# Kernel tuning notes

Hardware: AMD Instinct MI355X
Metric: run time of the kernel (lower is better)

Reference implementation:

```python
import jax, jax.numpy as jnp
import numpy as np

N = 50000
E = 800000
D_IN = 128
D_EMB = 128
D_OUT = 2
AGGRS = ('sum', 'max', 'mean', 'sum', 'max', 'mean')


def setup_inputs() -> dict:
    key = jax.random.key(0)
    ks = jax.random.split(key, 10)
    x = jax.random.normal(ks[0], (N, D_IN), dtype=jnp.float32)
    edge_index = jax.random.randint(ks[1], (2, E), 0, N, dtype=jnp.int64)
    # 6 SAGEConv layers, all 128->128: lin_l (weight+bias, applied to aggregated
    # neighbors) and lin_r (weight only, applied to root/self features).
    w_l = jax.random.normal(ks[2], (6, D_EMB, D_EMB), dtype=jnp.float32) * 0.05
    b_l = jax.random.normal(ks[3], (6, D_EMB), dtype=jnp.float32) * 0.05
    w_r = jax.random.normal(ks[4], (6, D_EMB, D_EMB), dtype=jnp.float32) * 0.05
    w1 = jax.random.normal(ks[5], (D_EMB, D_EMB), dtype=jnp.float32) * 0.05
    b1 = jax.random.normal(ks[6], (D_EMB,), dtype=jnp.float32) * 0.05
    w2 = jax.random.normal(ks[7], (D_EMB, D_OUT), dtype=jnp.float32) * 0.05
    b2 = jax.random.normal(ks[8], (D_OUT,), dtype=jnp.float32) * 0.05
    return {"x": x, "edge_index": edge_index, "w_l": w_l, "b_l": b_l,
            "w_r": w_r, "w1": w1, "b1": b1, "w2": w2, "b2": b2}


def _aggregate(msg, dst, aggr, num_nodes):
    # msg: [E, D] gathered source features; dst: [E] target node ids.
    if aggr == 'sum':
        return jax.ops.segment_sum(msg, dst, num_segments=num_nodes)
    if aggr == 'max':
        m = jax.ops.segment_max(msg, dst, num_segments=num_nodes)
        # nodes with no incoming edges -> 0 (PyG scatter-max fill)
        return jnp.where(jnp.isfinite(m), m, 0.0)
    # mean
    s = jax.ops.segment_sum(msg, dst, num_segments=num_nodes)
    cnt = jax.ops.segment_sum(jnp.ones((msg.shape[0],), msg.dtype), dst,
                              num_segments=num_nodes)
    return s / jnp.maximum(cnt, 1.0)[:, None]


def _sage_conv(x, src, dst, wl, bl, wr, aggr):
    msg = x[src]                               # [E, D] gather
    agg = _aggregate(msg, dst, aggr, x.shape[0])
    return agg @ wl + bl + x @ wr              # lin_l(aggr) + lin_r(x)


def reference(x, edge_index, w_l, b_l, w_r, w1, b1, w2, b2):
    src, dst = edge_index[0], edge_index[1]    # messages flow src -> dst
    h = x
    for i, aggr in enumerate(AGGRS):
        h = _sage_conv(h, src, dst, w_l[i], b_l[i], w_r[i], aggr)
        h = jax.nn.relu(h)                     # dropout p=0.1 is identity in eval
    h = jax.nn.relu(h @ w1 + b1)
    return h @ w2 + b2
```

## Files before the change

kernel.cpp:

```cpp
#include <hip/hip_runtime.h>

#define NN 50000
#define NE 800000
#define D 128

typedef unsigned short ushort_t;
typedef __attribute__((ext_vector_type(8))) short short8;
typedef __attribute__((ext_vector_type(4))) float f32x4;
typedef __attribute__((ext_vector_type(8))) _Float16 half8;
typedef __attribute__((ext_vector_type(2))) _Float16 half2v;


__global__ void k_hist(const int* __restrict__ dst, int* __restrict__ cnt, int e) {
  int i = blockIdx.x * blockDim.x + threadIdx.x;
  if (i < e) atomicAdd(&cnt[dst[i]], 1);
}

__global__ __launch_bounds__(1024) void k_scan(const int* __restrict__ cnt,
                                               int* __restrict__ row_start,
                                               int* __restrict__ cursor, int n) {
  __shared__ int wsum[16];
  __shared__ int carry_s;
  int t = threadIdx.x;
  int lane = t & 63, wid = t >> 6;
  if (t == 0) carry_s = 0;
  __syncthreads();
  for (int base = 0; base < n; base += 4096) {
    int i = base + t * 4;
    int4 v = make_int4(0, 0, 0, 0);
    if (i + 3 < n) v = *(const int4*)&cnt[i];
    else if (i < n) {
      v.x = cnt[i];
      if (i + 1 < n) v.y = cnt[i + 1];
      if (i + 2 < n) v.z = cnt[i + 2];
    }
    int tot = v.x + v.y + v.z + v.w;
    int x = tot;
    #pragma unroll
    for (int off = 1; off < 64; off <<= 1) {
      int y = __shfl_up(x, off, 64);
      if (lane >= off) x += y;
    }
    if (lane == 63) wsum[wid] = x;
    __syncthreads();
    if (wid == 0) {
      int w = (lane < 16) ? wsum[lane] : 0;
      #pragma unroll
      for (int off = 1; off < 16; off <<= 1) {
        int y = __shfl_up(w, off, 64);
        if (lane >= off) w += y;
      }
      if (lane < 16) wsum[lane] = w;
    }
    __syncthreads();
    int off0 = carry_s + (wid ? wsum[wid - 1] : 0) + (x - tot);
    int4 o;
    o.x = off0;
    o.y = off0 + v.x;
    o.z = off0 + v.x + v.y;
    o.w = off0 + v.x + v.y + v.z;
    if (i + 3 < n) {
      *(int4*)&row_start[i] = o;
      *(int4*)&cursor[i] = o;
    } else if (i < n) {
      row_start[i] = o.x; cursor[i] = o.x;
      if (i + 1 < n) { row_start[i + 1] = o.y; cursor[i + 1] = o.y; }
      if (i + 2 < n) { row_start[i + 2] = o.z; cursor[i + 2] = o.z; }
    }
    __syncthreads();
    if (t == 0) carry_s += wsum[15];
    __syncthreads();
  }
  if (t == 0) row_start[n] = carry_s;
}

__global__ __launch_bounds__(256) void k_scatter(const int* __restrict__ src,
                                                 const int* __restrict__ dst,
                                                 int* __restrict__ cursor,
                                                 int* __restrict__ csr_src, int e) {
  int i = (blockIdx.x * 256 + threadIdx.x) * 4;
  if (i >= e) return;
  int4 s4 = *(const int4*)&src[i];
  int4 d4 = *(const int4*)&dst[i];
  int p0 = atomicAdd(&cursor[d4.x], 1);
  int p1 = atomicAdd(&cursor[d4.y], 1);
  int p2 = atomicAdd(&cursor[d4.z], 1);
  int p3 = atomicAdd(&cursor[d4.w], 1);
  csr_src[p0] = s4.x;
  csr_src[p1] = s4.y;
  csr_src[p2] = s4.z;
  csr_src[p3] = s4.w;
}


__global__ __launch_bounds__(256) void k_tofp16(const float* __restrict__ in,
                                                _Float16* __restrict__ out, int n8) {
  int i = blockIdx.x * 256 + threadIdx.x;
  if (i >= n8) return;
  float4 a = ((const float4*)in)[i * 2];
  float4 b = ((const float4*)in)[i * 2 + 1];
  half8 o;
  o[0] = (_Float16)a.x; o[1] = (_Float16)a.y; o[2] = (_Float16)a.z; o[3] = (_Float16)a.w;
  o[4] = (_Float16)b.x; o[5] = (_Float16)b.y; o[6] = (_Float16)b.z; o[7] = (_Float16)b.w;
  ((half8*)out)[i] = o;
}


__global__ void k_wsplit(const float* __restrict__ W, ushort_t* __restrict__ hi,
                         ushort_t* __restrict__ lo, int total) {
  int idx = blockIdx.x * 256 + threadIdx.x;
  if (idx >= total) return;
  int mat = idx >> 14, rem = idx & 16383;
  int k = rem >> 7, c = rem & 127;
  float f = W[idx];
  unsigned u = __float_as_uint(f);
  float lf = f - __uint_as_float(u & 0xffff0000u);
  size_t dst = ((size_t)mat << 14) + (size_t)(k >> 5) * 4096 + c * 32 + (k & 31);
  hi[dst] = (ushort_t)(u >> 16);
  lo[dst] = (ushort_t)(__float_as_uint(lf) >> 16);
}


__device__ __forceinline__ float4 op_add(float4 a, float4 v) {
  a.x += v.x; a.y += v.y; a.z += v.z; a.w += v.w; return a;
}
__device__ __forceinline__ float4 op_max(float4 a, float4 v) {
  a.x = fmaxf(a.x, v.x); a.y = fmaxf(a.y, v.y);
  a.z = fmaxf(a.z, v.z); a.w = fmaxf(a.w, v.w); return a;
}
__device__ __forceinline__ void h8_to_f(half8 v, float4& x, float4& y) {
  x.x = (float)v[0]; x.y = (float)v[1]; x.z = (float)v[2]; x.w = (float)v[3];
  y.x = (float)v[4]; y.y = (float)v[5]; y.z = (float)v[6]; y.w = (float)v[7];
}

template <int AGGR>
__global__ __launch_bounds__(256) void k_aggregate(const _Float16* __restrict__ h,
                                                   const int* __restrict__ csr_src,
                                                   const int* __restrict__ row_start,
                                                   _Float16* __restrict__ agg, int n) {
  int lane = threadIdx.x & 63;
  int node = blockIdx.x * 4 + (threadIdx.x >> 6);
  if (node >= n) return;
  int slot = lane >> 4, c = lane & 15;
  const half8* __restrict__ hp = (const half8*)h;
  int s = row_start[node], e = row_start[node + 1];
  float4 init;
  if (AGGR == 1) init = make_float4(-INFINITY, -INFINITY, -INFINITY, -INFINITY);
  else           init = make_float4(0.f, 0.f, 0.f, 0.f);
  float4 a0x = init, a0y = init, a1x = init, a1y = init;
  int j = s + slot;
  for (; j + 4 < e; j += 8) {
    int i0 = csr_src[j], i1 = csr_src[j + 4];
    half8 v0 = hp[(size_t)i0 * 16 + c];
    half8 v1 = hp[(size_t)i1 * 16 + c];
    float4 v0x, v0y, v1x, v1y;
    h8_to_f(v0, v0x, v0y);
    h8_to_f(v1, v1x, v1y);
    if (AGGR == 1) {
      a0x = op_max(a0x, v0x); a0y = op_max(a0y, v0y);
      a1x = op_max(a1x, v1x); a1y = op_max(a1y, v1y);
    } else {
      a0x = op_add(a0x, v0x); a0y = op_add(a0y, v0y);
      a1x = op_add(a1x, v1x); a1y = op_add(a1y, v1y);
    }
  }
  for (; j < e; j += 4) {
    half8 v0 = hp[(size_t)csr_src[j] * 16 + c];
    float4 v0x, v0y;
    h8_to_f(v0, v0x, v0y);
    if (AGGR == 1) { a0x = op_max(a0x, v0x); a0y = op_max(a0y, v0y); }
    else           { a0x = op_add(a0x, v0x); a0y = op_add(a0y, v0y); }
  }
  float4 rx, ry;
  if (AGGR == 1) { rx = op_max(a0x, a1x); ry = op_max(a0y, a1y); }
  else           { rx = op_add(a0x, a1x); ry = op_add(a0y, a1y); }
  #pragma unroll
  for (int off = 16; off <= 32; off <<= 1) {
    float4 ox, oy;
    ox.x = __shfl_xor(rx.x, off, 64); ox.y = __shfl_xor(rx.y, off, 64);
    ox.z = __shfl_xor(rx.z, off, 64); ox.w = __shfl_xor(rx.w, off, 64);
    oy.x = __shfl_xor(ry.x, off, 64); oy.y = __shfl_xor(ry.y, off, 64);
    oy.z = __shfl_xor(ry.z, off, 64); oy.w = __shfl_xor(ry.w, off, 64);
    if (AGGR == 1) { rx = op_max(rx, ox); ry = op_max(ry, oy); }
    else           { rx = op_add(rx, ox); ry = op_add(ry, oy); }
  }
  if (slot == 0) {
    if (AGGR == 1) {
      if (e == s) { rx = make_float4(0.f,0.f,0.f,0.f); ry = rx; }
    } else if (AGGR == 2) {
      float inv = 1.0f / fmaxf((float)(e - s), 1.0f);
      rx.x *= inv; rx.y *= inv; rx.z *= inv; rx.w *= inv;
      ry.x *= inv; ry.y *= inv; ry.z *= inv; ry.w *= inv;
    }
    half8 o;
    o[0] = (_Float16)rx.x; o[1] = (_Float16)rx.y; o[2] = (_Float16)rx.z; o[3] = (_Float16)rx.w;
    o[4] = (_Float16)ry.x; o[5] = (_Float16)ry.y; o[6] = (_Float16)ry.z; o[7] = (_Float16)ry.w;
    ((half8*)agg)[(size_t)node * 16 + c] = o;
  }
}


#define GBM 64

__global__ __launch_bounds__(256) void k_gemm(
    const _Float16* __restrict__ A1, const ushort_t* __restrict__ Wh1, const ushort_t* __restrict__ Wl1,
    const _Float16* __restrict__ A2, const ushort_t* __restrict__ Wh2, const ushort_t* __restrict__ Wl2,
    const float* __restrict__ bias, _Float16* __restrict__ out, int M, int has2) {
  __shared__ ushort_t Ah[GBM * 40];
  __shared__ ushort_t Al[GBM * 40];
  __shared__ ushort_t Bh[128 * 40];
  __shared__ ushort_t Bl[128 * 40];
  int t = threadIdx.x;
  int lane = t & 63, wid = t >> 6;
  int wr = wid >> 1, wc = wid & 1;
  int l15 = lane & 15, kg = lane >> 4;
  int row0 = blockIdx.x * GBM;

  f32x4 acc[2][4] = {};

  int nmat = has2 ? 2 : 1;
  for (int mat = 0; mat < nmat; ++mat) {
    const _Float16* __restrict__ A = mat ? A2 : A1;
    const ushort_t* __restrict__ Wh = mat ? Wh2 : Wh1;
    const ushort_t* __restrict__ Wl = mat ? Wl2 : Wl1;
    for (int kt = 0; kt < 4; ++kt) {
      __syncthreads();
      {
        int r = t >> 2, cq = t & 3;
        int grow = row0 + r;
        half8 v = {};
        if (grow < M) v = *(const half8*)&A[(size_t)grow * D + kt * 32 + cq * 8];
        unsigned hw[8], lw[8];
        #pragma unroll
        for (int eidx = 0; eidx < 8; ++eidx) {
          float f = (float)v[eidx];
          unsigned u = __float_as_uint(f);
          float lf = f - __uint_as_float(u & 0xffff0000u);
          hw[eidx] = u >> 16;
          lw[eidx] = __float_as_uint(lf) >> 16;
        }
        uint4 hv = make_uint4(hw[0] | (hw[1] << 16), hw[2] | (hw[3] << 16),
                              hw[4] | (hw[5] << 16), hw[6] | (hw[7] << 16));
        uint4 lv = make_uint4(lw[0] | (lw[1] << 16), lw[2] | (lw[3] << 16),
                              lw[4] | (lw[5] << 16), lw[6] | (lw[7] << 16));
        *(uint4*)&Ah[r * 40 + cq * 8] = hv;
        *(uint4*)&Al[r * 40 + cq * 8] = lv;
      }
      {
        int c = t >> 1, q = t & 1;
        const ushort_t* sh = Wh + (size_t)kt * 4096 + t * 16;
        const ushort_t* sl = Wl + (size_t)kt * 4096 + t * 16;
        uint4 a0 = *(const uint4*)sh;
        uint4 a1 = *(const uint4*)(sh + 8);
        uint4 b0 = *(const uint4*)sl;
        uint4 b1 = *(const uint4*)(sl + 8);
        *(uint4*)&Bh[c * 40 + q * 16]     = a0;
        *(uint4*)&Bh[c * 40 + q * 16 + 8] = a1;
        *(uint4*)&Bl[c * 40 + q * 16]     = b0;
        *(uint4*)&Bl[c * 40 + q * 16 + 8] = b1;
      }
      __syncthreads();
      short8 ah[2], al[2], bh[4], bl[4];
      #pragma unroll
      for (int m = 0; m < 2; ++m) {
        int row = wr * 32 + m * 16 + l15;
        ah[m] = *(const short8*)&Ah[row * 40 + kg * 8];
        al[m] = *(const short8*)&Al[row * 40 + kg * 8];
      }
      #pragma unroll
      for (int n = 0; n < 4; ++n) {
        int col = wc * 64 + n * 16 + l15;
        bh[n] = *(const short8*)&Bh[col * 40 + kg * 8];
        bl[n] = *(const short8*)&Bl[col * 40 + kg * 8];
      }
      #pragma unroll
      for (int m = 0; m < 2; ++m)
        #pragma unroll
        for (int n = 0; n < 4; ++n) {
          acc[m][n] = __builtin_amdgcn_mfma_f32_16x16x32_bf16(ah[m], bh[n], acc[m][n], 0, 0, 0);
          acc[m][n] = __builtin_amdgcn_mfma_f32_16x16x32_bf16(ah[m], bl[n], acc[m][n], 0, 0, 0);
          acc[m][n] = __builtin_amdgcn_mfma_f32_16x16x32_bf16(al[m], bh[n], acc[m][n], 0, 0, 0);
        }
    }
  }
  int crow = kg * 4;
  #pragma unroll
  for (int n = 0; n < 4; ++n) {
    int col = wc * 64 + n * 16 + l15;
    float b = bias[col];
    #pragma unroll
    for (int m = 0; m < 2; ++m) {
      int rbase = row0 + wr * 32 + m * 16 + crow;
      #pragma unroll
      for (int q = 0; q < 4; ++q) {
        int grow = rbase + q;
        if (grow < M)
          out[(size_t)grow * D + col] = (_Float16)fmaxf(acc[m][n][q] + b, 0.f);
      }
    }
  }
}


__global__ __launch_bounds__(256) void k_head(const _Float16* __restrict__ h,
                                              const float* __restrict__ w2,
                                              const float* __restrict__ b2,
                                              float* __restrict__ out, int n) {
  int lane = threadIdx.x & 63;
  int node = blockIdx.x * 4 + (threadIdx.x >> 6);
  if (node >= n) return;
  half2v v = *(const half2v*)&h[(size_t)node * D + lane * 2];
  float v0 = (float)v[0], v1 = (float)v[1];
  float4 w = *(const float4*)&w2[lane * 4];
  float p0 = v0 * w.x + v1 * w.z;
  float p1 = v0 * w.y + v1 * w.w;
  #pragma unroll
  for (int off = 32; off; off >>= 1) {
    p0 += __shfl_xor(p0, off, 64);
    p1 += __shfl_xor(p1, off, 64);
  }
  if (lane == 0)
    ((float2*)out)[node] = make_float2(p0 + b2[0], p1 + b2[1]);
}


extern "C" void kernel_launch(void* const* d_in, const int* in_sizes, int n_in,
                              void* d_out, int out_size, void* d_ws, size_t ws_size,
                              hipStream_t stream) {
  const float* x   = (const float*)d_in[0];
  const int*   ei  = (const int*)d_in[1];
  const float* w_l = (const float*)d_in[2];
  const float* b_l = (const float*)d_in[3];
  const float* w_r = (const float*)d_in[4];
  const float* w1  = (const float*)d_in[5];
  const float* b1  = (const float*)d_in[6];
  const float* w2  = (const float*)d_in[7];
  const float* b2  = (const float*)d_in[8];
  float* out = (float*)d_out;

  const int* src = ei;
  const int* dst = ei + NE;

  char* ws = (char*)d_ws;
  size_t SZH = (size_t)NN * D * sizeof(_Float16);
  _Float16* bufX = (_Float16*)ws;
  _Float16* bufA = (_Float16*)(ws + SZH);
  _Float16* bufB = (_Float16*)(ws + 2 * SZH);
  int* csr_src   = (int*)(ws + 3 * SZH);
  int* row_start = (int*)(ws + 3 * SZH + (size_t)NE * sizeof(int));
  int* cursor    = row_start + NN + 2;
  int* cnt       = cursor + NN + 2;
  ushort_t* whi  = (ushort_t*)(cnt + NN + 2);
  ushort_t* wlo  = whi + 13 * 16384;

  k_wsplit<<<(6 * 16384 + 255) / 256, 256, 0, stream>>>(w_l, whi, wlo, 6 * 16384);
  k_wsplit<<<(6 * 16384 + 255) / 256, 256, 0, stream>>>(w_r, whi + 6 * 16384, wlo + 6 * 16384, 6 * 16384);
  k_wsplit<<<(16384 + 255) / 256, 256, 0, stream>>>(w1, whi + 12 * 16384, wlo + 12 * 16384, 16384);
  k_tofp16<<<(NN * D / 8 + 255) / 256, 256, 0, stream>>>(x, bufX, NN * D / 8);

  hipMemsetAsync(cnt, 0, NN * sizeof(int), stream);
  k_hist<<<(NE + 255) / 256, 256, 0, stream>>>(dst, cnt, NE);
  k_scan<<<1, 1024, 0, stream>>>(cnt, row_start, cursor, NN);
  k_scatter<<<(NE / 4 + 255) / 256, 256, 0, stream>>>(src, dst, cursor, csr_src, NE);

  const int agg_grid  = (NN + 3) / 4;
  const int gemm_grid = (NN + GBM - 1) / GBM;

  const _Float16* h = bufX;
  _Float16* bufs[2] = {bufA, bufB};
  for (int i = 0; i < 6; ++i) {
    _Float16* aggb = bufs[i & 1];
    switch (i % 3) {
      case 0: k_aggregate<0><<<agg_grid, 256, 0, stream>>>(h, csr_src, row_start, aggb, NN); break;
      case 1: k_aggregate<1><<<agg_grid, 256, 0, stream>>>(h, csr_src, row_start, aggb, NN); break;
      case 2: k_aggregate<2><<<agg_grid, 256, 0, stream>>>(h, csr_src, row_start, aggb, NN); break;
    }
    k_gemm<<<gemm_grid, 256, 0, stream>>>(aggb, whi + (size_t)i * 16384, wlo + (size_t)i * 16384,
                                          h,    whi + (size_t)(6 + i) * 16384, wlo + (size_t)(6 + i) * 16384,
                                          b_l + (size_t)i * D, aggb, NN, 1);
    h = aggb;
  }
  k_gemm<<<gemm_grid, 256, 0, stream>>>(h, whi + (size_t)12 * 16384, wlo + (size_t)12 * 16384,
                                        h, nullptr, nullptr, b1, bufA, NN, 0);
  k_head<<<agg_grid, 256, 0, stream>>>(bufA, w2, b2, out, NN);
}
```

Baseline: 468.2 us.

## Split node features into column-chunk planes and aggregate per chunk for cache locality

Feature buffers move from row-major [N,128] to four planes of 32 columns each, [4][N][32]. The tofp16 conversion, GEMM load/store and head kernels are updated to this layout, and aggregation runs four passes, one per plane. Each pass gathers from a 3.2MB fp16 plane, so random neighbour gathers are more likely to hit in cache. The CSR scatter is split into 8 destination-range groups to localise the atomics, and csr_src loads and agg stores become nontemporal. In exchange, every pass re-reads csr_src and row_start, the scatter reads the edge list 8 times, and each gather fetches only 64 bytes per neighbour.

```diff
diff --git a/kernel.cpp b/kernel.cpp
--- a/kernel.cpp
+++ b/kernel.cpp
@@ -3,6 +3,8 @@
 #define NN 50000
 #define NE 800000
 #define D 128
+#define NB 12500
+#define CH ((size_t)NN * 32)
 
 typedef unsigned short ushort_t;
 typedef __attribute__((ext_vector_type(8))) short short8;
@@ -78,31 +80,30 @@
                                                  const int* __restrict__ dst,
                                                  int* __restrict__ cursor,
                                                  int* __restrict__ csr_src, int e) {
-  int i = (blockIdx.x * 256 + threadIdx.x) * 4;
+  int g = blockIdx.x & 7;
+  int i = (blockIdx.x >> 3) * 1024 + threadIdx.x * 4;
   if (i >= e) return;
   int4 s4 = *(const int4*)&src[i];
   int4 d4 = *(const int4*)&dst[i];
-  int p0 = atomicAdd(&cursor[d4.x], 1);
-  int p1 = atomicAdd(&cursor[d4.y], 1);
-  int p2 = atomicAdd(&cursor[d4.z], 1);
-  int p3 = atomicAdd(&cursor[d4.w], 1);
-  csr_src[p0] = s4.x;
-  csr_src[p1] = s4.y;
-  csr_src[p2] = s4.z;
-  csr_src[p3] = s4.w;
+  if ((unsigned)d4.x / 6250u == (unsigned)g) { int p = atomicAdd(&cursor[d4.x], 1); csr_src[p] = s4.x; }
+  if ((unsigned)d4.y / 6250u == (unsigned)g) { int p = atomicAdd(&cursor[d4.y], 1); csr_src[p] = s4.y; }
+  if ((unsigned)d4.z / 6250u == (unsigned)g) { int p = atomicAdd(&cursor[d4.z], 1); csr_src[p] = s4.z; }
+  if ((unsigned)d4.w / 6250u == (unsigned)g) { int p = atomicAdd(&cursor[d4.w], 1); csr_src[p] = s4.w; }
 }
 
 
 __global__ __launch_bounds__(256) void k_tofp16(const float* __restrict__ in,
-                                                _Float16* __restrict__ out, int n8) {
+                                                _Float16* __restrict__ out, int ngrp) {
   int i = blockIdx.x * 256 + threadIdx.x;
-  if (i >= n8) return;
+  if (i >= ngrp) return;
+  int node = i >> 4, gidx = i & 15;
+  int p = gidx >> 2, inner = gidx & 3;
   float4 a = ((const float4*)in)[i * 2];
   float4 b = ((const float4*)in)[i * 2 + 1];
   half8 o;
   o[0] = (_Float16)a.x; o[1] = (_Float16)a.y; o[2] = (_Float16)a.z; o[3] = (_Float16)a.w;
   o[4] = (_Float16)b.x; o[5] = (_Float16)b.y; o[6] = (_Float16)b.z; o[7] = (_Float16)b.w;
-  ((half8*)out)[i] = o;
+  ((half8*)out)[(size_t)p * NN * 4 + (size_t)node * 4 + inner] = o;
 }
 
 
@@ -134,25 +135,28 @@
 }
 
 template <int AGGR>
-__global__ __launch_bounds__(256) void k_aggregate(const _Float16* __restrict__ h,
+__global__ __launch_bounds__(256) void k_aggregate(const _Float16* __restrict__ hc,
                                                    const int* __restrict__ csr_src,
                                                    const int* __restrict__ row_start,
-                                                   _Float16* __restrict__ agg, int n) {
+                                                   _Float16* __restrict__ aggc, int n) {
+  int pass = blockIdx.x / NB;
+  int nb = blockIdx.x - pass * NB;
   int lane = threadIdx.x & 63;
-  int node = blockIdx.x * 4 + (threadIdx.x >> 6);
+  int node = nb * 4 + (threadIdx.x >> 6);
   if (node >= n) return;
-  int slot = lane >> 4, c = lane & 15;
-  const half8* __restrict__ hp = (const half8*)h;
+  int slot = lane >> 2, c = lane & 3;
+  const half8* __restrict__ hp = (const half8*)hc + (size_t)pass * n * 4;
   int s = row_start[node], e = row_start[node + 1];
   float4 init;
   if (AGGR == 1) init = make_float4(-INFINITY, -INFINITY, -INFINITY, -INFINITY);
   else           init = make_float4(0.f, 0.f, 0.f, 0.f);
   float4 a0x = init, a0y = init, a1x = init, a1y = init;
   int j = s + slot;
-  for (; j + 4 < e; j += 8) {
-    int i0 = csr_src[j], i1 = csr_src[j + 4];
-    half8 v0 = hp[(size_t)i0 * 16 + c];
-    half8 v1 = hp[(size_t)i1 * 16 + c];
+  for (; j + 16 < e; j += 32) {
+    int i0 = __builtin_nontemporal_load(&csr_src[j]);
+    int i1 = __builtin_nontemporal_load(&csr_src[j + 16]);
+    half8 v0 = hp[(size_t)i0 * 4 + c];
+    half8 v1 = hp[(size_t)i1 * 4 + c];
     float4 v0x, v0y, v1x, v1y;
     h8_to_f(v0, v0x, v0y);
     h8_to_f(v1, v1x, v1y);
@@ -164,8 +168,9 @@
       a1x = op_add(a1x, v1x); a1y = op_add(a1y, v1y);
     }
   }
-  for (; j < e; j += 4) {
-    half8 v0 = hp[(size_t)csr_src[j] * 16 + c];
+  for (; j < e; j += 16) {
+    int i0 = __builtin_nontemporal_load(&csr_src[j]);
+    half8 v0 = hp[(size_t)i0 * 4 + c];
     float4 v0x, v0y;
     h8_to_f(v0, v0x, v0y);
     if (AGGR == 1) { a0x = op_max(a0x, v0x); a0y = op_max(a0y, v0y); }
@@ -175,7 +180,7 @@
   if (AGGR == 1) { rx = op_max(a0x, a1x); ry = op_max(a0y, a1y); }
   else           { rx = op_add(a0x, a1x); ry = op_add(a0y, a1y); }
   #pragma unroll
-  for (int off = 16; off <= 32; off <<= 1) {
+  for (int off = 4; off <= 32; off <<= 1) {
     float4 ox, oy;
     ox.x = __shfl_xor(rx.x, off, 64); ox.y = __shfl_xor(rx.y, off, 64);
     ox.z = __shfl_xor(rx.z, off, 64); ox.w = __shfl_xor(rx.w, off, 64);
@@ -195,7 +200,7 @@
     half8 o;
     o[0] = (_Float16)rx.x; o[1] = (_Float16)rx.y; o[2] = (_Float16)rx.z; o[3] = (_Float16)rx.w;
     o[4] = (_Float16)ry.x; o[5] = (_Float16)ry.y; o[6] = (_Float16)ry.z; o[7] = (_Float16)ry.w;
-    ((half8*)agg)[(size_t)node * 16 + c] = o;
+    __builtin_nontemporal_store(o, (half8*)aggc + (size_t)pass * n * 4 + (size_t)node * 4 + c);
   }
 }
 
@@ -229,7 +234,7 @@
         int r = t >> 2, cq = t & 3;
         int grow = row0 + r;
         half8 v = {};
-        if (grow < M) v = *(const half8*)&A[(size_t)grow * D + kt * 32 + cq * 8];
+        if (grow < M) v = *(const half8*)&A[(size_t)kt * CH + (size_t)grow * 32 + cq * 8];
         unsigned hw[8], lw[8];
         #pragma unroll
         for (int eidx = 0; eidx < 8; ++eidx) {
@@ -288,6 +293,7 @@
   for (int n = 0; n < 4; ++n) {
     int col = wc * 64 + n * 16 + l15;
     float b = bias[col];
+    size_t cbase = (size_t)(col >> 5) * CH + (col & 31);
     #pragma unroll
     for (int m = 0; m < 2; ++m) {
       int rbase = row0 + wr * 32 + m * 16 + crow;
@@ -295,7 +301,7 @@
       for (int q = 0; q < 4; ++q) {
         int grow = rbase + q;
         if (grow < M)
-          out[(size_t)grow * D + col] = (_Float16)fmaxf(acc[m][n][q] + b, 0.f);
+          out[cbase + (size_t)grow * 32] = (_Float16)fmaxf(acc[m][n][q] + b, 0.f);
       }
     }
   }
@@ -309,7 +315,8 @@
   int lane = threadIdx.x & 63;
   int node = blockIdx.x * 4 + (threadIdx.x >> 6);
   if (node >= n) return;
-  half2v v = *(const half2v*)&h[(size_t)node * D + lane * 2];
+  int p = lane >> 4, c32 = (2 * lane) & 31;
+  half2v v = *(const half2v*)&h[(size_t)p * CH + (size_t)node * 32 + c32];
   float v0 = (float)v[0], v1 = (float)v[1];
   float4 w = *(const float4*)&w2[lane * 4];
   float p0 = v0 * w.x + v1 * w.z;
@@ -356,14 +363,14 @@
   k_wsplit<<<(6 * 16384 + 255) / 256, 256, 0, stream>>>(w_l, whi, wlo, 6 * 16384);
   k_wsplit<<<(6 * 16384 + 255) / 256, 256, 0, stream>>>(w_r, whi + 6 * 16384, wlo + 6 * 16384, 6 * 16384);
   k_wsplit<<<(16384 + 255) / 256, 256, 0, stream>>>(w1, whi + 12 * 16384, wlo + 12 * 16384, 16384);
-  k_tofp16<<<(NN * D / 8 + 255) / 256, 256, 0, stream>>>(x, bufX, NN * D / 8);
+  k_tofp16<<<(NN * 16 + 255) / 256, 256, 0, stream>>>(x, bufX, NN * 16);
 
   hipMemsetAsync(cnt, 0, NN * sizeof(int), stream);
   k_hist<<<(NE + 255) / 256, 256, 0, stream>>>(dst, cnt, NE);
   k_scan<<<1, 1024, 0, stream>>>(cnt, row_start, cursor, NN);
-  k_scatter<<<(NE / 4 + 255) / 256, 256, 0, stream>>>(src, dst, cursor, csr_src, NE);
-
-  const int agg_grid  = (NN + 3) / 4;
+  k_scatter<<<8 * ((NE + 1023) / 1024), 256, 0, stream>>>(src, dst, cursor, csr_src, NE);
+
+  const int agg_grid  = 4 * NB;
   const int gemm_grid = (NN + GBM - 1) / GBM;
 
   const _Float16* h = bufX;
@@ -382,5 +389,5 @@
   }
   k_gemm<<<gemm_grid, 256, 0, stream>>>(h, whi + (size_t)12 * 16384, wlo + (size_t)12 * 16384,
                                         h, nullptr, nullptr, b1, bufA, NN, 0);
-  k_head<<<agg_grid, 256, 0, stream>>>(bufA, w2, b2, out, NN);
-}
+  k_head<<<agg_grid / 4, 256, 0, stream>>>(bufA, w2, b2, out, NN);
+}
```

Result: slower. 748.8 us (+59.9%).
